# Performance work log

Hardware: AMD Instinct MI355X
Metric: run time of the kernel (lower is better)

Reference implementation:

```python
import jax, jax.numpy as jnp
import numpy as np

D_MODEL = 256
NHEAD = 8
DHEAD = D_MODEL // NHEAD
LN_EPS = 1e-5
ATTN_EPS = 1e-6


def layer_norm(x, gamma, beta):
    mu = jnp.mean(x, axis=-1, keepdims=True)
    var = jnp.mean(jnp.square(x - mu), axis=-1, keepdims=True)
    return (x - mu) * jax.lax.rsqrt(var + LN_EPS) * gamma + beta


def setup_inputs() -> dict:
    key = jax.random.key(0)
    ks = jax.random.split(key, 12)
    B, L, S = 8, 4096, 4096
    s = 1.0 / np.sqrt(D_MODEL)
    return {
        "x": jax.random.normal(ks[0], (B, L, D_MODEL), jnp.float32),
        "source": jax.random.normal(ks[1], (B, S, D_MODEL), jnp.float32),
        "wq": jax.random.normal(ks[2], (D_MODEL, D_MODEL), jnp.float32) * s,
        "wk": jax.random.normal(ks[3], (D_MODEL, D_MODEL), jnp.float32) * s,
        "wv": jax.random.normal(ks[4], (D_MODEL, D_MODEL), jnp.float32) * s,
        "wmerge": jax.random.normal(ks[5], (D_MODEL, D_MODEL), jnp.float32) * s,
        "w1": jax.random.normal(ks[6], (2 * D_MODEL, D_MODEL), jnp.float32) * s,
        "w2": jax.random.normal(ks[7], (D_MODEL, 2 * D_MODEL), jnp.float32) * (1.0 / np.sqrt(2 * D_MODEL)),
        "g1": jnp.ones((D_MODEL,), jnp.float32),
        "b1": jnp.zeros((D_MODEL,), jnp.float32),
        "g2": jnp.ones((D_MODEL,), jnp.float32),
        "b2": jnp.zeros((D_MODEL,), jnp.float32),
    }


def reference(x, source, wq, wk, wv, wmerge, w1, w2, g1, b1, g2, b2):
    B, L, _ = x.shape
    S = source.shape[1]
    # QKV projections (bias-free Linear: y = x @ W^T), split into heads
    q = (x @ wq.T).reshape(B, L, NHEAD, DHEAD)
    k = (source @ wk.T).reshape(B, S, NHEAD, DHEAD)
    v = (source @ wv.T).reshape(B, S, NHEAD, DHEAD)
    # LinearAttention (LoFTR): feature map elu(.)+1, kernelized attention
    Q = jax.nn.elu(q) + 1.0
    K = jax.nn.elu(k) + 1.0
    v_len = jnp.asarray(S, v.dtype)
    values = v / v_len
    KV = jnp.einsum('bshd,bshv->bhdv', K, values)        # [B,H,D,D]
    Z = 1.0 / (jnp.einsum('blhd,bhd->blh', Q, K.sum(axis=1)) + ATTN_EPS)
    attended = jnp.einsum('blhd,bhdv,blh->blhv', Q, KV, Z) * v_len
    # merge + residual LN
    message = attended.reshape(B, L, D_MODEL) @ wmerge.T
    x = x + layer_norm(message, g1, b1)
    # MLP (d -> 2d -> d, ReLU) + residual LN
    h = jax.nn.relu(x @ w1.T) @ w2.T
    x = x + layer_norm(h, g2, b2)
    return x
```

## Files before the change

kernel.cpp:

```cpp
#include <hip/hip_runtime.h>

#define DM 256
#define SEQ 4096
#define XSTR 528
#define KSTR 144

typedef __attribute__((ext_vector_type(8))) short bf16x8;
typedef __attribute__((ext_vector_type(4))) float f32x4;

#define MFMA16(a, b, c) __builtin_amdgcn_mfma_f32_16x16x32_bf16(a, b, c, 0, 0, 0)

__device__ __forceinline__ short f2bf(float f) {
    union { float f; unsigned u; } c; c.f = f;
    unsigned r = (c.u + 0x7FFFu + ((c.u >> 16) & 1u)) >> 16;
    return (short)r;
}
__device__ __forceinline__ float bf2f(short s) {
    union { unsigned u; float f; } c; c.u = ((unsigned)(unsigned short)s) << 16; return c.f;
}
__device__ __forceinline__ bf16x8 pack8(float4 a, float4 b) {
    bf16x8 r;
    r[0] = f2bf(a.x); r[1] = f2bf(a.y); r[2] = f2bf(a.z); r[3] = f2bf(a.w);
    r[4] = f2bf(b.x); r[5] = f2bf(b.y); r[6] = f2bf(b.z); r[7] = f2bf(b.w);
    return r;
}

__global__ __launch_bounds__(256) void kWconv(const float* __restrict__ wq, const float* __restrict__ wk,
                                              const float* __restrict__ wv, const float* __restrict__ wm,
                                              const float* __restrict__ w1, const float* __restrict__ w2,
                                              short* __restrict__ dstws) {
    int blk = blockIdx.x;
    const float* src; short* dst;
    if (blk < 32)       { src = wq; dst = dstws;          }
    else if (blk < 64)  { src = wk; dst = dstws + 65536;  blk -= 32; }
    else if (blk < 96)  { src = wv; dst = dstws + 131072; blk -= 64; }
    else if (blk < 128) { src = wm; dst = dstws + 196608; blk -= 96; }
    else if (blk < 192) { src = w1; dst = dstws + 262144; blk -= 128; }
    else                { src = w2; dst = dstws + 393216; blk -= 192; }
    int idx = (blk * 256 + threadIdx.x) * 8;
    float4 f0 = *(const float4*)(src + idx), f1 = *(const float4*)(src + idx + 4);
    *(bf16x8*)(dst + idx) = pack8(f0, f1);
}

__global__ __launch_bounds__(512, 4) void kA(const float* __restrict__ src,
                                             const short* __restrict__ wk, const short* __restrict__ wv,
                                             short* __restrict__ kv_part, float* __restrict__ ksum_part) {
    __shared__ char lds[73728];
    int t = threadIdx.x, lane = t & 63, w = t >> 6, r16 = lane & 15, g = lane >> 4;
    int b = blockIdx.x >> 6, blk = blockIdx.x & 63;
    const float* S = src + ((size_t)b * SEQ + blk * 64) * DM;
#pragma unroll
    for (int i = 0; i < 4; i++) {
        int chunk = t + i * 512, row = chunk >> 5, c8 = chunk & 31;
        const float* p = S + row * DM + c8 * 8;
        float4 f0 = *(const float4*)p, f1 = *(const float4*)(p + 4);
        *(bf16x8*)(lds + row * XSTR + c8 * 16) = pack8(f0, f1);
    }
    __syncthreads();
    f32x4 zz = {0.f, 0.f, 0.f, 0.f};
    f32x4 ak[4][2], av[4][2];
#pragma unroll
    for (int mi = 0; mi < 4; mi++)
#pragma unroll
        for (int ni = 0; ni < 2; ni++) { ak[mi][ni] = zz; av[mi][ni] = zz; }
    const char* aB0 = lds + r16 * XSTR + g * 16;
    const short* wkB0 = wk + (w * 32 + r16) * DM + g * 8;
    const short* wvB0 = wv + (w * 32 + r16) * DM + g * 8;
#pragma unroll
    for (int kt = 0; kt < 8; kt++) {
        bf16x8 A[4];
#pragma unroll
        for (int mi = 0; mi < 4; mi++)
            A[mi] = *(const bf16x8*)(aB0 + mi * (16 * XSTR) + kt * 64);
#pragma unroll
        for (int ni = 0; ni < 2; ni++) {
            bf16x8 Bk = *(const bf16x8*)(wkB0 + ni * (16 * DM) + kt * 32);
            bf16x8 Bv = *(const bf16x8*)(wvB0 + ni * (16 * DM) + kt * 32);
#pragma unroll
            for (int mi = 0; mi < 4; mi++) {
                ak[mi][ni] = MFMA16(A[mi], Bk, ak[mi][ni]);
                av[mi][ni] = MFMA16(A[mi], Bv, av[mi][ni]);
            }
        }
    }
    __syncthreads();
    char* kT = lds + w * 9216;
    char* vT = kT + 4608;
    float ksp[2] = {0.f, 0.f};
#pragma unroll
    for (int mi = 0; mi < 4; mi++)
#pragma unroll
        for (int ni = 0; ni < 2; ni++)
#pragma unroll
            for (int j = 0; j < 4; j++) {
                float q = ak[mi][ni][j];
                float e = q > 0.f ? q + 1.f : __expf(q);
                ksp[ni] += e;
                int srow = mi * 16 + g * 4 + j, feat = ni * 16 + r16;
                int by = feat * KSTR + srow * 2;
                *(short*)(kT + by) = f2bf(e);
                *(short*)(vT + by) = f2bf(av[mi][ni][j]);
            }
    __syncthreads();
    f32x4 kv[2][2];
#pragma unroll
    for (int vi = 0; vi < 2; vi++)
#pragma unroll
        for (int di = 0; di < 2; di++) kv[vi][di] = zz;
    {
        const char* vB = vT + r16 * KSTR + g * 16;
        const char* kB = kT + r16 * KSTR + g * 16;
#pragma unroll
        for (int st = 0; st < 2; st++) {
            bf16x8 Af[2], Bf[2];
#pragma unroll
            for (int vi = 0; vi < 2; vi++) {
                Af[vi] = *(const bf16x8*)(vB + vi * (16 * KSTR) + st * 64);
                Bf[vi] = *(const bf16x8*)(kB + vi * (16 * KSTR) + st * 64);
            }
#pragma unroll
            for (int vi = 0; vi < 2; vi++)
#pragma unroll
                for (int di = 0; di < 2; di++) kv[vi][di] = MFMA16(Af[vi], Bf[di], kv[vi][di]);
        }
    }
    short* kvp = kv_part + ((size_t)(b * 64 + blk) * 8 + w) * 1024;
#pragma unroll
    for (int vi = 0; vi < 2; vi++)
#pragma unroll
        for (int di = 0; di < 2; di++)
#pragma unroll
            for (int j = 0; j < 4; j++) {
                int v = vi * 16 + g * 4 + j, d = di * 16 + r16;
                kvp[v * 32 + d] = f2bf(kv[vi][di][j]);
            }
#pragma unroll
    for (int ni = 0; ni < 2; ni++) {
        ksp[ni] += __shfl_xor(ksp[ni], 16);
        ksp[ni] += __shfl_xor(ksp[ni], 32);
    }
    if (lane < 16) {
        float* kp = ksum_part + (size_t)(b * 64 + blk) * 256 + w * 32;
#pragma unroll
        for (int ni = 0; ni < 2; ni++) kp[ni * 16 + lane] = ksp[ni];
    }
}

__global__ __launch_bounds__(256) void kA2(const short* __restrict__ kv_part, const float* __restrict__ ksum_part,
                                           short* __restrict__ kvt_bf, float* __restrict__ ksum4) {
    int blk = blockIdx.x, t = threadIdx.x;
    int b = blk >> 5, h = (blk >> 2) & 7, q = blk & 3;
    int e = q * 256 + t;
    float s0 = 0.f, s1 = 0.f, s2 = 0.f, s3 = 0.f;
    for (int bk = 0; bk < 64; bk += 4) {
        s0 += bf2f(kv_part[((size_t)(b * 64 + bk) * 8 + h) * 1024 + e]);
        s1 += bf2f(kv_part[((size_t)(b * 64 + bk + 1) * 8 + h) * 1024 + e]);
        s2 += bf2f(kv_part[((size_t)(b * 64 + bk + 2) * 8 + h) * 1024 + e]);
        s3 += bf2f(kv_part[((size_t)(b * 64 + bk + 3) * 8 + h) * 1024 + e]);
    }
    kvt_bf[(size_t)(b * 8 + h) * 1024 + e] = f2bf((s0 + s1) + (s2 + s3));
    if (t < 32) {
        float s = 0.f;
        for (int bk = q * 16; bk < q * 16 + 16; bk++)
            s += ksum_part[(size_t)(b * 64 + bk) * 256 + h * 32 + t];
        ksum4[((b * 8 + h) * 4 + q) * 32 + t] = s;
    }
}

__global__ __launch_bounds__(512, 4) void kBC(const float* __restrict__ x,
                                              const short* __restrict__ wq_bf, const short* __restrict__ wm_bf,
                                              const short* __restrict__ w1_bf, const short* __restrict__ w2_bf,
                                              const short* __restrict__ kvt_bf, const float* __restrict__ ksum4,
                                              const float* __restrict__ g1, const float* __restrict__ b1,
                                              const float* __restrict__ g2, const float* __restrict__ b2,
                                              float* __restrict__ out) {
    __shared__ char lds[72704];
    char* xt = lds;
    char* qa = lds + 33792;
    float* red = (float*)(lds + 67584);
    float* ksl = (float*)(lds + 71680);
    int t = threadIdx.x, lane = t & 63, w = t >> 6, r16 = lane & 15, g = lane >> 4;
    int b = blockIdx.x >> 6, lb = blockIdx.x & 63, l0 = lb * 64;
    const float* xb = x + ((size_t)b * SEQ + l0) * DM;
#pragma unroll
    for (int i = 0; i < 4; i++) {
        int chunk = t + i * 512, row = chunk >> 5, c8 = chunk & 31;
        const float* p = xb + row * DM + c8 * 8;
        float4 f0 = *(const float4*)p, f1 = *(const float4*)(p + 4);
        *(bf16x8*)(xt + row * XSTR + c8 * 16) = pack8(f0, f1);
    }
    if (t < 256) {
        int h = t >> 5, d = t & 31;
        const float* kp = ksum4 + (size_t)((b * 8 + h) * 4) * 32 + d;
        ksl[t] = (kp[0] + kp[32]) + (kp[64] + kp[96]);
    }
    __syncthreads();
    f32x4 zz = {0.f, 0.f, 0.f, 0.f};
    const char* aXB = xt + r16 * XSTR + g * 16;
    const char* aQB = qa + r16 * XSTR + g * 16;
    f32x4 acc[4][2];
#pragma unroll
    for (int mi = 0; mi < 4; mi++)
#pragma unroll
        for (int ni = 0; ni < 2; ni++) acc[mi][ni] = zz;
    {
        const short* wqB = wq_bf + (w * 32 + r16) * DM + g * 8;
#pragma unroll
        for (int kt = 0; kt < 8; kt++) {
            bf16x8 A[4], Bf[2];
#pragma unroll
            for (int mi = 0; mi < 4; mi++)
                A[mi] = *(const bf16x8*)(aXB + mi * (16 * XSTR) + kt * 64);
#pragma unroll
            for (int ni = 0; ni < 2; ni++)
                Bf[ni] = *(const bf16x8*)(wqB + ni * (16 * DM) + kt * 32);
#pragma unroll
            for (int mi = 0; mi < 4; mi++)
#pragma unroll
                for (int ni = 0; ni < 2; ni++) acc[mi][ni] = MFMA16(A[mi], Bf[ni], acc[mi][ni]);
        }
    }
    float ks0 = ksl[w * 32 + r16], ks1 = ksl[w * 32 + 16 + r16];
    float Zr[4][4];
#pragma unroll
    for (int mi = 0; mi < 4; mi++)
#pragma unroll
        for (int j = 0; j < 4; j++) {
#pragma unroll
            for (int ni = 0; ni < 2; ni++) {
                float q = acc[mi][ni][j];
                acc[mi][ni][j] = q > 0.f ? q + 1.f : __expf(q);
            }
            float d0 = acc[mi][0][j] * ks0 + acc[mi][1][j] * ks1;
#pragma unroll
            for (int m = 1; m < 16; m <<= 1) d0 += __shfl_xor(d0, m);
            Zr[mi][j] = 1.f / (d0 + 1e-6f);
        }
#pragma unroll
    for (int mi = 0; mi < 4; mi++)
#pragma unroll
        for (int ni = 0; ni < 2; ni++)
#pragma unroll
            for (int j = 0; j < 4; j++) {
                int row = mi * 16 + g * 4 + j, col = w * 32 + ni * 16 + r16;
                *(short*)(qa + row * XSTR + col * 2) = f2bf(acc[mi][ni][j]);
            }
    f32x4 at[4][2];
#pragma unroll
    for (int mi = 0; mi < 4; mi++)
#pragma unroll
        for (int vi = 0; vi < 2; vi++) at[mi][vi] = zz;
    {
        bf16x8 A2[4], B2[2];
#pragma unroll
        for (int mi = 0; mi < 4; mi++)
            A2[mi] = *(const bf16x8*)(qa + (mi * 16 + r16) * XSTR + (w * 32 + g * 8) * 2);
        const short* kvb = kvt_bf + (size_t)(b * 8 + w) * 1024;
#pragma unroll
        for (int vi = 0; vi < 2; vi++)
            B2[vi] = *(const bf16x8*)(kvb + (vi * 16 + r16) * 32 + g * 8);
#pragma unroll
        for (int mi = 0; mi < 4; mi++)
#pragma unroll
            for (int vi = 0; vi < 2; vi++) at[mi][vi] = MFMA16(A2[mi], B2[vi], at[mi][vi]);
    }
#pragma unroll
    for (int mi = 0; mi < 4; mi++)
#pragma unroll
        for (int vi = 0; vi < 2; vi++)
#pragma unroll
            for (int j = 0; j < 4; j++) {
                int row = mi * 16 + g * 4 + j, col = w * 32 + vi * 16 + r16;
                *(short*)(qa + row * XSTR + col * 2) = f2bf(at[mi][vi][j] * Zr[mi][j]);
            }
    __syncthreads();
    f32x4 am[4][2];
#pragma unroll
    for (int mi = 0; mi < 4; mi++)
#pragma unroll
        for (int ni = 0; ni < 2; ni++) am[mi][ni] = zz;
    {
        const short* wmB = wm_bf + (w * 32 + r16) * DM + g * 8;
#pragma unroll
        for (int kt = 0; kt < 8; kt++) {
            bf16x8 A[4], Bf[2];
#pragma unroll
            for (int mi = 0; mi < 4; mi++)
                A[mi] = *(const bf16x8*)(aQB + mi * (16 * XSTR) + kt * 64);
#pragma unroll
            for (int ni = 0; ni < 2; ni++)
                Bf[ni] = *(const bf16x8*)(wmB + ni * (16 * DM) + kt * 32);
#pragma unroll
            for (int mi = 0; mi < 4; mi++)
#pragma unroll
                for (int ni = 0; ni < 2; ni++) am[mi][ni] = MFMA16(A[mi], Bf[ni], am[mi][ni]);
        }
    }
#pragma unroll
    for (int mi = 0; mi < 4; mi++)
#pragma unroll
        for (int j = 0; j < 4; j++) {
            float s = am[mi][0][j] + am[mi][1][j];
            float s2 = am[mi][0][j] * am[mi][0][j] + am[mi][1][j] * am[mi][1][j];
#pragma unroll
            for (int m = 1; m < 16; m <<= 1) { s += __shfl_xor(s, m); s2 += __shfl_xor(s2, m); }
            if (r16 == 0) { int row = mi * 16 + g * 4 + j; red[(row * 8 + w) * 2] = s; red[(row * 8 + w) * 2 + 1] = s2; }
        }
    __syncthreads();
    {
        float g1v[2], b1v[2];
#pragma unroll
        for (int ni = 0; ni < 2; ni++) { int col = w * 32 + ni * 16 + r16; g1v[ni] = g1[col]; b1v[ni] = b1[col]; }
#pragma unroll
        for (int mi = 0; mi < 4; mi++)
#pragma unroll
            for (int j = 0; j < 4; j++) {
                int row = mi * 16 + g * 4 + j;
                float mu = 0.f, ex2 = 0.f;
#pragma unroll
                for (int ww = 0; ww < 8; ww++) { mu += red[(row * 8 + ww) * 2]; ex2 += red[(row * 8 + ww) * 2 + 1]; }
                mu *= (1.f / DM); ex2 *= (1.f / DM);
                float rstd = rsqrtf(ex2 - mu * mu + 1e-5f);
#pragma unroll
                for (int ni = 0; ni < 2; ni++) {
                    int col = w * 32 + ni * 16 + r16;
                    char* bp = xt + row * XSTR + col * 2;
                    float xv = bf2f(*(const short*)bp);
                    *(short*)bp = f2bf(xv + (am[mi][ni][j] - mu) * rstd * g1v[ni] + b1v[ni]);
                }
            }
    }
    __syncthreads();
    f32x4 a2[4][2];
#pragma unroll
    for (int mi = 0; mi < 4; mi++)
#pragma unroll
        for (int ni = 0; ni < 2; ni++) a2[mi][ni] = zz;
#pragma unroll
    for (int hf = 0; hf < 2; hf++) {
        f32x4 a1[4][2];
#pragma unroll
        for (int mi = 0; mi < 4; mi++)
#pragma unroll
            for (int ni = 0; ni < 2; ni++) a1[mi][ni] = zz;
        {
            const short* w1B = w1_bf + (hf * 256 + w * 32 + r16) * DM + g * 8;
#pragma unroll
            for (int kt = 0; kt < 8; kt++) {
                bf16x8 A[4], Bf[2];
#pragma unroll
                for (int mi = 0; mi < 4; mi++)
                    A[mi] = *(const bf16x8*)(aXB + mi * (16 * XSTR) + kt * 64);
#pragma unroll
                for (int ni = 0; ni < 2; ni++)
                    Bf[ni] = *(const bf16x8*)(w1B + ni * (16 * DM) + kt * 32);
#pragma unroll
                for (int mi = 0; mi < 4; mi++)
#pragma unroll
                    for (int ni = 0; ni < 2; ni++) a1[mi][ni] = MFMA16(A[mi], Bf[ni], a1[mi][ni]);
            }
        }
#pragma unroll
        for (int mi = 0; mi < 4; mi++)
#pragma unroll
            for (int ni = 0; ni < 2; ni++)
#pragma unroll
                for (int j = 0; j < 4; j++) {
                    float hv = a1[mi][ni][j]; hv = hv > 0.f ? hv : 0.f;
                    int row = mi * 16 + g * 4 + j, col = w * 32 + ni * 16 + r16;
                    *(short*)(qa + row * XSTR + col * 2) = f2bf(hv);
                }
        __syncthreads();
        {
            const short* w2B = w2_bf + (w * 32 + r16) * 512 + hf * 256 + g * 8;
#pragma unroll
            for (int kt = 0; kt < 8; kt++) {
                bf16x8 A[4], Bf[2];
#pragma unroll
                for (int mi = 0; mi < 4; mi++)
                    A[mi] = *(const bf16x8*)(aQB + mi * (16 * XSTR) + kt * 64);
#pragma unroll
                for (int ni = 0; ni < 2; ni++)
                    Bf[ni] = *(const bf16x8*)(w2B + ni * (16 * 512) + kt * 32);
#pragma unroll
                for (int mi = 0; mi < 4; mi++)
#pragma unroll
                    for (int ni = 0; ni < 2; ni++) a2[mi][ni] = MFMA16(A[mi], Bf[ni], a2[mi][ni]);
            }
        }
        __syncthreads();
    }
#pragma unroll
    for (int mi = 0; mi < 4; mi++)
#pragma unroll
        for (int j = 0; j < 4; j++) {
            float s = a2[mi][0][j] + a2[mi][1][j];
            float s2 = a2[mi][0][j] * a2[mi][0][j] + a2[mi][1][j] * a2[mi][1][j];
#pragma unroll
            for (int m = 1; m < 16; m <<= 1) { s += __shfl_xor(s, m); s2 += __shfl_xor(s2, m); }
            if (r16 == 0) { int row = mi * 16 + g * 4 + j; red[(row * 8 + w) * 2] = s; red[(row * 8 + w) * 2 + 1] = s2; }
        }
    __syncthreads();
    {
        float g2v[2], b2v[2];
#pragma unroll
        for (int ni = 0; ni < 2; ni++) { int col = w * 32 + ni * 16 + r16; g2v[ni] = g2[col]; b2v[ni] = b2[col]; }
        float* op = out + ((size_t)b * SEQ + l0) * DM;
#pragma unroll
        for (int mi = 0; mi < 4; mi++)
#pragma unroll
            for (int j = 0; j < 4; j++) {
                int row = mi * 16 + g * 4 + j;
                float mu = 0.f, ex2 = 0.f;
#pragma unroll
                for (int ww = 0; ww < 8; ww++) { mu += red[(row * 8 + ww) * 2]; ex2 += red[(row * 8 + ww) * 2 + 1]; }
                mu *= (1.f / DM); ex2 *= (1.f / DM);
                float rstd = rsqrtf(ex2 - mu * mu + 1e-5f);
#pragma unroll
                for (int ni = 0; ni < 2; ni++) {
                    int col = w * 32 + ni * 16 + r16;
                    float xv = bf2f(*(const short*)(xt + row * XSTR + col * 2));
                    op[row * DM + col] = xv + (a2[mi][ni][j] - mu) * rstd * g2v[ni] + b2v[ni];
                }
            }
    }
}

extern "C" void kernel_launch(void* const* d_in, const int* in_sizes, int n_in,
                              void* d_out, int out_size, void* d_ws, size_t ws_size,
                              hipStream_t stream) {
    const float* x   = (const float*)d_in[0];
    const float* src = (const float*)d_in[1];
    const float* wq  = (const float*)d_in[2];
    const float* wk  = (const float*)d_in[3];
    const float* wv  = (const float*)d_in[4];
    const float* wm  = (const float*)d_in[5];
    const float* w1  = (const float*)d_in[6];
    const float* w2  = (const float*)d_in[7];
    const float* g1  = (const float*)d_in[8];
    const float* b1  = (const float*)d_in[9];
    const float* g2  = (const float*)d_in[10];
    const float* b2  = (const float*)d_in[11];
    float* out = (float*)d_out;

    char* ws = (char*)d_ws;
    short* w_bf      = (short*)ws;
    short* kvt_bf    = (short*)(ws + 1048576);
    float* ksum4     = (float*)(ws + 1179648);
    short* kv_part   = (short*)(ws + 1212416);
    float* ksum_part = (float*)(ws + 9601024);

    kWconv<<<256, 256, 0, stream>>>(wq, wk, wv, wm, w1, w2, w_bf);
    kA<<<512, 512, 0, stream>>>(src, w_bf + 65536, w_bf + 131072, kv_part, ksum_part);
    kA2<<<256, 256, 0, stream>>>(kv_part, ksum_part, kvt_bf, ksum4);
    kBC<<<512, 512, 0, stream>>>(x, w_bf, w_bf + 196608, w_bf + 262144, w_bf + 393216,
                                 kvt_bf, ksum4, g1, b1, g2, b2, out);
}
```

Baseline: 215.6 us.

## Replace KV partial-sum reduction kernel with float atomics into workspace

Removes the separate kA2 reduction kernel. Each kA block now atomically adds its fp32 KV and K-sum partials straight into a single accumulator per batch and head, and kWconv zeroes that accumulator first. kBC reads the fp32 KV, converts it to bf16 in registers, and reads the K-sum directly. This drops one launch and the bf16 partial buffer round trip, at the cost of 64-way atomic contention per address and a non-deterministic summation order. The bf16 conversion helper is also switched to the HIP intrinsic.

Result: no change. 218.0 us (+1.1%).

```diff
diff --git a/kernel.cpp b/kernel.cpp
--- a/kernel.cpp
+++ b/kernel.cpp
@@ -1,4 +1,5 @@
 #include <hip/hip_runtime.h>
+#include <hip/hip_bf16.h>
 
 #define DM 256
 #define SEQ 4096
@@ -11,9 +12,9 @@
 #define MFMA16(a, b, c) __builtin_amdgcn_mfma_f32_16x16x32_bf16(a, b, c, 0, 0, 0)
 
 __device__ __forceinline__ short f2bf(float f) {
-    union { float f; unsigned u; } c; c.f = f;
-    unsigned r = (c.u + 0x7FFFu + ((c.u >> 16) & 1u)) >> 16;
-    return (short)r;
+    union { __hip_bfloat16 h; short s; } u;
+    u.h = __float2bfloat16(f);
+    return u.s;
 }
 __device__ __forceinline__ float bf2f(short s) {
     union { unsigned u; float f; } c; c.u = ((unsigned)(unsigned short)s) << 16; return c.f;
@@ -28,8 +29,12 @@
 __global__ __launch_bounds__(256) void kWconv(const float* __restrict__ wq, const float* __restrict__ wk,
                                               const float* __restrict__ wv, const float* __restrict__ wm,
                                               const float* __restrict__ w1, const float* __restrict__ w2,
-                                              short* __restrict__ dstws) {
+                                              short* __restrict__ dstws, float* __restrict__ kva,
+                                              float* __restrict__ ksum) {
     int blk = blockIdx.x;
+    int gid = blk * 256 + threadIdx.x;
+    kva[gid] = 0.f;
+    if (gid < 2048) ksum[gid] = 0.f;
     const float* src; short* dst;
     if (blk < 32)       { src = wq; dst = dstws;          }
     else if (blk < 64)  { src = wk; dst = dstws + 65536;  blk -= 32; }
@@ -44,7 +49,7 @@
 
 __global__ __launch_bounds__(512, 4) void kA(const float* __restrict__ src,
                                              const short* __restrict__ wk, const short* __restrict__ wv,
-                                             short* __restrict__ kv_part, float* __restrict__ ksum_part) {
+                                             float* __restrict__ kva, float* __restrict__ ksum) {
     __shared__ char lds[73728];
     int t = threadIdx.x, lane = t & 63, w = t >> 6, r16 = lane & 15, g = lane >> 4;
     int b = blockIdx.x >> 6, blk = blockIdx.x & 63;
@@ -124,7 +129,7 @@
                 for (int di = 0; di < 2; di++) kv[vi][di] = MFMA16(Af[vi], Bf[di], kv[vi][di]);
         }
     }
-    short* kvp = kv_part + ((size_t)(b * 64 + blk) * 8 + w) * 1024;
+    float* kvp = kva + (size_t)(b * 8 + w) * 1024;
 #pragma unroll
     for (int vi = 0; vi < 2; vi++)
 #pragma unroll
@@ -132,7 +137,7 @@
 #pragma unroll
             for (int j = 0; j < 4; j++) {
                 int v = vi * 16 + g * 4 + j, d = di * 16 + r16;
-                kvp[v * 32 + d] = f2bf(kv[vi][di][j]);
+                atomicAdd(&kvp[v * 32 + d], kv[vi][di][j]);
             }
 #pragma unroll
     for (int ni = 0; ni < 2; ni++) {
@@ -140,37 +145,16 @@
         ksp[ni] += __shfl_xor(ksp[ni], 32);
     }
     if (lane < 16) {
-        float* kp = ksum_part + (size_t)(b * 64 + blk) * 256 + w * 32;
-#pragma unroll
-        for (int ni = 0; ni < 2; ni++) kp[ni * 16 + lane] = ksp[ni];
-    }
-}
-
-__global__ __launch_bounds__(256) void kA2(const short* __restrict__ kv_part, const float* __restrict__ ksum_part,
-                                           short* __restrict__ kvt_bf, float* __restrict__ ksum4) {
-    int blk = blockIdx.x, t = threadIdx.x;
-    int b = blk >> 5, h = (blk >> 2) & 7, q = blk & 3;
-    int e = q * 256 + t;
-    float s0 = 0.f, s1 = 0.f, s2 = 0.f, s3 = 0.f;
-    for (int bk = 0; bk < 64; bk += 4) {
-        s0 += bf2f(kv_part[((size_t)(b * 64 + bk) * 8 + h) * 1024 + e]);
-        s1 += bf2f(kv_part[((size_t)(b * 64 + bk + 1) * 8 + h) * 1024 + e]);
-        s2 += bf2f(kv_part[((size_t)(b * 64 + bk + 2) * 8 + h) * 1024 + e]);
-        s3 += bf2f(kv_part[((size_t)(b * 64 + bk + 3) * 8 + h) * 1024 + e]);
-    }
-    kvt_bf[(size_t)(b * 8 + h) * 1024 + e] = f2bf((s0 + s1) + (s2 + s3));
-    if (t < 32) {
-        float s = 0.f;
-        for (int bk = q * 16; bk < q * 16 + 16; bk++)
-            s += ksum_part[(size_t)(b * 64 + bk) * 256 + h * 32 + t];
-        ksum4[((b * 8 + h) * 4 + q) * 32 + t] = s;
+#pragma unroll
+        for (int ni = 0; ni < 2; ni++)
+            atomicAdd(&ksum[(b * 8 + w) * 32 + ni * 16 + lane], ksp[ni]);
     }
 }
 
 __global__ __launch_bounds__(512, 4) void kBC(const float* __restrict__ x,
                                               const short* __restrict__ wq_bf, const short* __restrict__ wm_bf,
                                               const short* __restrict__ w1_bf, const short* __restrict__ w2_bf,
-                                              const short* __restrict__ kvt_bf, const float* __restrict__ ksum4,
+                                              const float* __restrict__ kva, const float* __restrict__ ksum,
                                               const float* __restrict__ g1, const float* __restrict__ b1,
                                               const float* __restrict__ g2, const float* __restrict__ b2,
                                               float* __restrict__ out) {
@@ -189,11 +173,7 @@
         float4 f0 = *(const float4*)p, f1 = *(const float4*)(p + 4);
         *(bf16x8*)(xt + row * XSTR + c8 * 16) = pack8(f0, f1);
     }
-    if (t < 256) {
-        int h = t >> 5, d = t & 31;
-        const float* kp = ksum4 + (size_t)((b * 8 + h) * 4) * 32 + d;
-        ksl[t] = (kp[0] + kp[32]) + (kp[64] + kp[96]);
-    }
+    if (t < 256) ksl[t] = ksum[b * 256 + t];
     __syncthreads();
     f32x4 zz = {0.f, 0.f, 0.f, 0.f};
     const char* aXB = xt + r16 * XSTR + g * 16;
@@ -255,10 +235,13 @@
 #pragma unroll
         for (int mi = 0; mi < 4; mi++)
             A2[mi] = *(const bf16x8*)(qa + (mi * 16 + r16) * XSTR + (w * 32 + g * 8) * 2);
-        const short* kvb = kvt_bf + (size_t)(b * 8 + w) * 1024;
-#pragma unroll
-        for (int vi = 0; vi < 2; vi++)
-            B2[vi] = *(const bf16x8*)(kvb + (vi * 16 + r16) * 32 + g * 8);
+        const float* kvb = kva + (size_t)(b * 8 + w) * 1024;
+#pragma unroll
+        for (int vi = 0; vi < 2; vi++) {
+            const float* p = kvb + (vi * 16 + r16) * 32 + g * 8;
+            float4 f0 = *(const float4*)p, f1 = *(const float4*)(p + 4);
+            B2[vi] = pack8(f0, f1);
+        }
 #pragma unroll
         for (int mi = 0; mi < 4; mi++)
 #pragma unroll
@@ -444,15 +427,12 @@
     float* out = (float*)d_out;
 
     char* ws = (char*)d_ws;
-    short* w_bf      = (short*)ws;
-    short* kvt_bf    = (short*)(ws + 1048576);
-    float* ksum4     = (float*)(ws + 1179648);
-    short* kv_part   = (short*)(ws + 1212416);
-    float* ksum_part = (float*)(ws + 9601024);
-
-    kWconv<<<256, 256, 0, stream>>>(wq, wk, wv, wm, w1, w2, w_bf);
-    kA<<<512, 512, 0, stream>>>(src, w_bf + 65536, w_bf + 131072, kv_part, ksum_part);
-    kA2<<<256, 256, 0, stream>>>(kv_part, ksum_part, kvt_bf, ksum4);
+    short* w_bf = (short*)ws;
+    float* kva  = (float*)(ws + 1048576);
+    float* ksum = (float*)(ws + 1310720);
+
+    kWconv<<<256, 256, 0, stream>>>(wq, wk, wv, wm, w1, w2, w_bf, kva, ksum);
+    kA<<<512, 512, 0, stream>>>(src, w_bf + 65536, w_bf + 131072, kva, ksum);
     kBC<<<512, 512, 0, stream>>>(x, w_bf, w_bf + 196608, w_bf + 262144, w_bf + 393216,
-                                 kvt_bf, ksum4, g1, b1, g2, b2, out);
-}
+                                 kva, ksum, g1, b1, g2, b2, out);
+}
```
